# Performance work log

Hardware: AMD Instinct MI355X
Metric: run time of the kernel (lower is better)

Reference implementation:

```python
import jax, jax.numpy as jnp
import numpy as np
from jax import lax

B, E, D, N, R, K = 4, 768, 1536, 16, 48, 4
H, W = 16, 16
L = H * W
NDIR = 4


def _perms():
    idx = np.arange(L)
    idx_v = np.arange(L).reshape(H, W).T.reshape(-1)  # column-major (vertical) scan order
    perms = [idx, idx[::-1].copy(), idx_v, idx_v[::-1].copy()]
    invs = [np.argsort(p) for p in perms]
    return [jnp.asarray(p) for p in perms], [jnp.asarray(p) for p in invs]

PERMS, INVS = _perms()


def setup_inputs() -> dict:
    key = jax.random.key(0)
    ks = jax.random.split(key, 10)
    hidden_states = jax.random.normal(ks[0], (B, L, E), jnp.float32)
    in_proj_w = jax.random.normal(ks[1], (2 * D, E), jnp.float32) * 0.02
    out_proj_w = jax.random.normal(ks[2], (E, D), jnp.float32) * 0.02
    conv_w = jax.random.normal(ks[3], (NDIR, D, K), jnp.float32) * 0.1
    conv_b = jax.random.normal(ks[4], (NDIR, D), jnp.float32) * 0.1
    xproj_w = jax.random.normal(ks[5], (NDIR, R + 2 * N, D), jnp.float32) * 0.02
    dt_init_std = R ** -0.5
    dtproj_w = jax.random.uniform(ks[6], (NDIR, D, R), jnp.float32, -dt_init_std, dt_init_std)
    dt = jnp.exp(jax.random.uniform(ks[7], (NDIR, D), jnp.float32)
                 * (np.log(0.1) - np.log(0.001)) + np.log(0.001))
    dt = jnp.clip(dt, 1e-4, None)
    dtproj_b = dt + jnp.log(-jnp.expm1(-dt))  # inverse-softplus init as in the module
    A_log = jnp.broadcast_to(
        jnp.log(jnp.arange(1, N + 1, dtype=jnp.float32))[None, None, :], (NDIR, D, N)).copy()
    D_param = jnp.ones((NDIR, D), jnp.float32)
    return dict(hidden_states=hidden_states, in_proj_w=in_proj_w, out_proj_w=out_proj_w,
                conv_w=conv_w, conv_b=conv_b, xproj_w=xproj_w, dtproj_w=dtproj_w,
                dtproj_b=dtproj_b, A_log=A_log, D_param=D_param)


def _mamba_dir(xz, cw, cb, xw, dtw, dtb, a_log, dpar):
    # xz: (B, 2D, L) in this direction's scan order
    x, z = xz[:, :D], xz[:, D:]
    # causal depthwise conv1d + SiLU (mamba_inner_fn conv path)
    x = lax.conv_general_dilated(x, cw[:, None, :], (1,), [(K - 1, 0)],
                                 feature_group_count=D,
                                 dimension_numbers=('NCH', 'OIH', 'NCH'))
    x = jax.nn.silu(x + cb[None, :, None])
    # x_proj -> dt, B, C
    x_dbl = jnp.einsum('bdl,kd->bkl', x, xw)
    dt, Bm, Cm = x_dbl[:, :R], x_dbl[:, R:R + N], x_dbl[:, R + N:]
    delta = jax.nn.softplus(jnp.einsum('brl,dr->bdl', dt, dtw) + dtb[None, :, None])
    A = -jnp.exp(a_log)                                  # (D, N)
    dA = jnp.exp(jnp.einsum('bdl,dn->lbdn', delta, A))   # (L, B, D, N)
    dBu = jnp.einsum('bdl,bnl,bdl->lbdn', delta, Bm, x)  # delta * B * u

    def step(h, inp):
        da, dbu = inp
        h = da * h + dbu
        return h, h

    h0 = jnp.zeros((x.shape[0], D, N), x.dtype)
    _, hs = lax.scan(step, h0, (dA, dBu))                # (L, B, D, N)
    y = jnp.einsum('lbdn,bnl->bdl', hs, Cm) + dpar[None, :, None] * x
    return y * jax.nn.silu(z)                            # gate, (B, D, L)


def reference(hidden_states, in_proj_w, out_proj_w, conv_w, conv_b,
              xproj_w, dtproj_w, dtproj_b, A_log, D_param):
    xz = jnp.einsum('ble,fe->bfl', hidden_states, in_proj_w)  # (B, 2D, L)
    out = jnp.zeros((hidden_states.shape[0], D, L), hidden_states.dtype)
    for i in range(NDIR):  # fixed small set of structurally distinct scan directions
        xz_i = xz[:, :, PERMS[i]]
        y = _mamba_dir(xz_i, conv_w[i], conv_b[i], xproj_w[i], dtproj_w[i],
                       dtproj_b[i], A_log[i], D_param[i])
        out = out + y[:, :, INVS[i]]  # multi_reverse then sum-fusion
    return jnp.einsum('bdl,ed->ble', out, out_proj_w)
```

## Files before the change

### kernel.cpp

```cpp
#include <hip/hip_runtime.h>
#include <hip/hip_bf16.h>

#define BI   4
#define LI   256
#define EI   768
#define DI   1536
#define NI   16
#define RI   48
#define KI   4
#define NDIRS 4
#define F2D  3072
#define MROWS 1024
#define LOG2E 1.4426950408889634f
#define LN2   0.6931471805599453f

typedef float    floatx2 __attribute__((ext_vector_type(2)));
typedef float    floatx4 __attribute__((ext_vector_type(4)));
typedef _Float16 halfx2  __attribute__((ext_vector_type(2)));
typedef _Float16 halfx4  __attribute__((ext_vector_type(4)));
typedef _Float16 halfx8  __attribute__((ext_vector_type(8)));

typedef __attribute__((address_space(3))) unsigned lds_u32;
typedef __attribute__((address_space(1))) const unsigned glb_u32;

__device__ __forceinline__ void load16(const _Float16* g, _Float16* l) {
    __builtin_amdgcn_global_load_lds((glb_u32*)g, (lds_u32*)l, 16, 0, 0);
}

__device__ __forceinline__ int perm_idx(int dir, int j) {
    switch (dir) {
        case 0:  return j;
        case 1:  return 255 - j;
        case 2:  return ((j & 15) << 4) | (j >> 4);
        default: return 255 - (((j & 15) << 4) | (j >> 4));
    }
}

template<int CTRL>
__device__ __forceinline__ float dpp_add(float p) {
    int t = __builtin_amdgcn_update_dpp(0, __builtin_bit_cast(int, p),
                                        CTRL, 0xf, 0xf, true);
    return p + __builtin_bit_cast(float, t);
}
__device__ __forceinline__ float grp8_sum(float p) {
    p = dpp_add<0xB1>(p);
    p = dpp_add<0x4E>(p);
    p = dpp_add<0x141>(p);
    return p;
}

template<int BM, int BN, int WGN, int FM, int FN, int VM>
__device__ __forceinline__ void gemm_core(const _Float16* __restrict__ Ah,
                                          const _Float16* __restrict__ Al, int lda,
                                          const _Float16* __restrict__ Bh,
                                          const _Float16* __restrict__ Bl, int ldb,
                                          int nChunks, _Float16* smem,
                                          floatx4 (&acc)[FM][FN]) {
    const int tid = threadIdx.x, lane = tid & 63, wave = tid >> 6;
    const int wave_m = wave / WGN, wave_n = wave % WGN;
    const int rr = lane & 15, koff = (lane >> 4) * 8;
    const int arow = wave_m * FM * 16, brow = wave_n * FN * 16;
    constexpr int BUFSZ = (BM + BN) * 64;

    auto stage = [&](int c, int bf) {
        _Float16* sAh = smem + bf * BUFSZ;
        _Float16* sAl = sAh + BM * 32;
        _Float16* sBh = sAh + BM * 64;
        _Float16* sBl = sAh + BM * 64 + BN * 32;
        for (int idx = tid; idx < BM * 4; idx += 256) {
            int r = idx >> 2, s = (idx & 3) * 8;
            load16(Ah + (size_t)r * lda + c * 32 + s, sAh + idx * 8);
            load16(Al + (size_t)r * lda + c * 32 + s, sAl + idx * 8);
        }
        for (int idx = tid; idx < BN * 4; idx += 256) {
            int r = idx >> 2, s = (idx & 3) * 8;
            load16(Bh + (size_t)r * ldb + c * 32 + s, sBh + idx * 8);
            load16(Bl + (size_t)r * ldb + c * 32 + s, sBl + idx * 8);
        }
    };

    stage(0, 0);

    for (int c = 0; c < nChunks; ++c) {
        const int bf = c & 1;
        if (c + 1 < nChunks) {
            stage(c + 1, bf ^ 1);
            asm volatile("s_waitcnt vmcnt(%0)" :: "n"(VM) : "memory");
        } else {
            asm volatile("s_waitcnt vmcnt(0)" ::: "memory");
        }
        __builtin_amdgcn_s_barrier();

        const _Float16* sAh = smem + bf * BUFSZ;
        const _Float16* sAl = sAh + BM * 32;
        const _Float16* sBh = sAh + BM * 64;
        const _Float16* sBl = sAh + BM * 64 + BN * 32;
        halfx8 ahf[FM], alf[FM], bhf[FN], blf[FN];
        #pragma unroll
        for (int i = 0; i < FM; ++i) {
            ahf[i] = *(const halfx8*)(sAh + (arow + i * 16 + rr) * 32 + koff);
            alf[i] = *(const halfx8*)(sAl + (arow + i * 16 + rr) * 32 + koff);
        }
        #pragma unroll
        for (int j = 0; j < FN; ++j) {
            bhf[j] = *(const halfx8*)(sBh + (brow + j * 16 + rr) * 32 + koff);
            blf[j] = *(const halfx8*)(sBl + (brow + j * 16 + rr) * 32 + koff);
        }
        #pragma unroll
        for (int i = 0; i < FM; ++i)
            #pragma unroll
            for (int j = 0; j < FN; ++j) {
                acc[i][j] = __builtin_amdgcn_mfma_f32_16x16x32_f16(ahf[i], bhf[j], acc[i][j], 0, 0, 0);
                acc[i][j] = __builtin_amdgcn_mfma_f32_16x16x32_f16(ahf[i], blf[j], acc[i][j], 0, 0, 0);
                acc[i][j] = __builtin_amdgcn_mfma_f32_16x16x32_f16(alf[i], bhf[j], acc[i][j], 0, 0, 0);
            }
        asm volatile("s_waitcnt lgkmcnt(0)" ::: "memory");
        __builtin_amdgcn_s_barrier();
    }
}

__global__ __launch_bounds__(256) void k_splitall(
        const float* __restrict__ hs,  const float* __restrict__ wip,
        const float* __restrict__ wop, const float* __restrict__ xw,
        const float* __restrict__ dtw,
        _Float16* __restrict__ hsh,  _Float16* __restrict__ hsl,
        _Float16* __restrict__ wiph, _Float16* __restrict__ wipl,
        _Float16* __restrict__ woph, _Float16* __restrict__ wopl,
        _Float16* __restrict__ xwh,  _Float16* __restrict__ xwl,
        _Float16* __restrict__ dtwh, _Float16* __restrict__ dtwl) {
    int i4 = (blockIdx.x * 256 + threadIdx.x) * 4;
    floatx4 v;
    _Float16 *dh, *dl; int off;
    if (i4 < 786432)        { off = i4;           v = *(const floatx4*)(hs + off);  dh = hsh;  dl = hsl;  }
    else if (i4 < 3145728)  { off = i4 - 786432;  v = *(const floatx4*)(wip + off); dh = wiph; dl = wipl; }
    else if (i4 < 4325376)  { off = i4 - 3145728; v = *(const floatx4*)(wop + off); dh = woph; dl = wopl; }
    else if (i4 < 4816896)  { off = i4 - 4325376; v = *(const floatx4*)(xw + off);  dh = xwh;  dl = xwl;  }
    else {
        int t0 = i4 - 4816896;
        int col = t0 & 63, dr = t0 >> 6;
        floatx4 z = {0.f, 0.f, 0.f, 0.f};
        v = (col < 48) ? *(const floatx4*)(dtw + (size_t)dr * 48 + col) : z;
        dh = dtwh; dl = dtwl; off = t0;
    }
    halfx4 hh, hl;
    #pragma unroll
    for (int e = 0; e < 4; ++e) {
        _Float16 h = (_Float16)v[e];
        hh[e] = h; hl[e] = (_Float16)(v[e] - (float)h);
    }
    *(halfx4*)(dh + off) = hh;
    *(halfx4*)(dl + off) = hl;
}

__global__ __launch_bounds__(256) void k_inproj_t(const _Float16* __restrict__ Ah,
                                                  const _Float16* __restrict__ Al,
                                                  const _Float16* __restrict__ Bh,
                                                  const _Float16* __restrict__ Bl,
                                                  float* __restrict__ C) {
    __shared__ _Float16 smem[2 * 192 * 64];
    int row0 = blockIdx.x * 64, col0 = blockIdx.y * 128;
    floatx4 acc[2][4] = {};
    gemm_core<64, 128, 2, 2, 4, 6>(Ah + (size_t)row0 * EI, Al + (size_t)row0 * EI, EI,
                                   Bh + (size_t)col0 * EI, Bl + (size_t)col0 * EI, EI,
                                   24, smem, acc);
    int lane = threadIdx.x & 63, wave = threadIdx.x >> 6;
    int cc = lane & 15, q = lane >> 4;
    int rbase = row0 + (wave >> 1) * 32, cbase = col0 + (wave & 1) * 64;
    #pragma unroll
    for (int i = 0; i < 2; ++i)
        #pragma unroll
        for (int j = 0; j < 4; ++j)
            #pragma unroll
            for (int r = 0; r < 4; ++r)
                C[(size_t)(rbase + i * 16 + q * 4 + r) * F2D + cbase + j * 16 + cc] = acc[i][j][r];
}

__global__ __launch_bounds__(256) void k_outproj_t(const _Float16* __restrict__ Ah,
                                                   const _Float16* __restrict__ Al,
                                                   const _Float16* __restrict__ Bh,
                                                   const _Float16* __restrict__ Bl,
                                                   float* __restrict__ C) {
    __shared__ _Float16 smem[2 * 192 * 64];
    int row0 = blockIdx.x * 64, col0 = blockIdx.y * 128, k0 = blockIdx.z * 384;
    float* Cp = C + (size_t)blockIdx.z * MROWS * EI;
    floatx4 acc[2][4] = {};
    gemm_core<64, 128, 2, 2, 4, 6>(Ah + (size_t)row0 * DI + k0, Al + (size_t)row0 * DI + k0, DI,
                                   Bh + (size_t)col0 * DI + k0, Bl + (size_t)col0 * DI + k0, DI,
                                   12, smem, acc);
    int lane = threadIdx.x & 63, wave = threadIdx.x >> 6;
    int cc = lane & 15, q = lane >> 4;
    int rbase = row0 + (wave >> 1) * 32, cbase = col0 + (wave & 1) * 64;
    #pragma unroll
    for (int i = 0; i < 2; ++i)
        #pragma unroll
        for (int j = 0; j < 4; ++j)
            #pragma unroll
            for (int r = 0; r < 4; ++r)
                Cp[(size_t)(rbase + i * 16 + q * 4 + r) * EI + cbase + j * 16 + cc] = acc[i][j][r];
}

__global__ __launch_bounds__(256) void k_osum(const float* __restrict__ oacc,
                                              float* __restrict__ out) {
    int i4 = (blockIdx.x * 256 + threadIdx.x) * 4;
    const size_t S = (size_t)MROWS * EI;
    floatx4 s = *(const floatx4*)(oacc + i4) + *(const floatx4*)(oacc + S + i4) +
                *(const floatx4*)(oacc + 2 * S + i4) + *(const floatx4*)(oacc + 3 * S + i4);
    *(floatx4*)(out + i4) = s;
}

__global__ __launch_bounds__(256) void k_xdbl_t(const _Float16* __restrict__ xh,
                                                const _Float16* __restrict__ xl,
                                                const _Float16* __restrict__ xwh,
                                                const _Float16* __restrict__ xwl,
                                                float* __restrict__ C) {
    __shared__ _Float16 smem[2 * 144 * 64];
    int row0 = blockIdx.x * 64, dir = blockIdx.y, k0 = blockIdx.z * 192;
    float* Cp = C + (size_t)blockIdx.z * NDIRS * MROWS * 80;
    floatx4 acc[1][5] = {};
    const size_t abase = ((size_t)dir * MROWS + row0) * DI + k0;
    const size_t bbase = (size_t)dir * 80 * DI + k0;
    gemm_core<64, 80, 1, 1, 5, 4>(xh + abase, xl + abase, DI,
                                  xwh + bbase, xwl + bbase, DI, 6, smem, acc);
    int lane = threadIdx.x & 63, wave = threadIdx.x >> 6;
    int cc = lane & 15, q = lane >> 4;
    int rbase = row0 + wave * 16;
    #pragma unroll
    for (int j = 0; j < 5; ++j)
        #pragma unroll
        for (int r = 0; r < 4; ++r)
            Cp[((size_t)dir * MROWS + rbase + q * 4 + r) * 80 + j * 16 + cc] = acc[0][j][r];
}

__global__ __launch_bounds__(256) void k_xsplit(const float* __restrict__ acc,
                                                _Float16* __restrict__ dtqh,
                                                _Float16* __restrict__ dtql,
                                                float* __restrict__ BCm) {
    const size_t PS = (size_t)NDIRS * MROWS * 80;
    int idx = blockIdx.x * 256 + threadIdx.x;
    int dir = idx / (MROWS * 96);
    int rem = idx - dir * MROWS * 96;
    int row = rem / 96, col = rem - row * 96;
    size_t rbase = (size_t)dir * MROWS + row;
    auto sum8 = [&](int c) {
        size_t o = rbase * 80 + c;
        float s = 0.f;
        #pragma unroll
        for (int kp = 0; kp < 8; ++kp) s += acc[kp * PS + o];
        return s;
    };
    if (col < 64) {
        float v = (col < 48) ? sum8(col) : 0.f;
        _Float16 h = (_Float16)v;
        dtqh[rbase * 64 + col] = h;
        dtql[rbase * 64 + col] = (_Float16)(v - (float)h);
    } else if (col < 80) {
        int n = col - 64;
        BCm[rbase * 32 + (n >> 1) * 4 + (n & 1)] = sum8(48 + n);
    } else {
        int n = col - 80;
        BCm[rbase * 32 + (n >> 1) * 4 + 2 + (n & 1)] = sum8(64 + n);
    }
}

__global__ __launch_bounds__(512) void k_conv4(const float* __restrict__ xz,
                                               const float* __restrict__ cw,
                                               const float* __restrict__ cb,
                                               _Float16* __restrict__ xh,
                                               _Float16* __restrict__ xl) {
    const int b = blockIdx.y, d0 = blockIdx.x * 16;
    const int tid = threadIdx.x;
    __shared__ float sx[256][18];

    for (int i = tid; i < 1024; i += 512) {
        int row = i >> 2, c4 = (i & 3) * 4;
        size_t o = ((size_t)b * 256 + row) * F2D + d0 + c4;
        floatx4 v = *(const floatx4*)(xz + o);
        floatx2 v0 = {v[0], v[1]}, v1 = {v[2], v[3]};
        *(floatx2*)&sx[row][c4]     = v0;
        *(floatx2*)&sx[row][c4 + 2] = v1;
    }
    __syncthreads();

    const int dsub = tid & 15, lg = tid >> 4;
    const int d = d0 + dsub, j0 = lg * 8;
    #pragma unroll
    for (int dir = 0; dir < NDIRS; ++dir) {
        floatx4 w = *(const floatx4*)(cw + ((size_t)dir * DI + d) * KI);
        float bias = cb[(size_t)dir * DI + d];
        float xm3 = (j0 >= 3) ? sx[perm_idx(dir, j0 - 3)][dsub] : 0.f;
        float xm2 = (j0 >= 2) ? sx[perm_idx(dir, j0 - 2)][dsub] : 0.f;
        float xm1 = (j0 >= 1) ? sx[perm_idx(dir, j0 - 1)][dsub] : 0.f;
        #pragma unroll
        for (int j = 0; j < 8; ++j) {
            float cur = sx[perm_idx(dir, j0 + j)][dsub];
            float s = bias + w[0] * xm3 + w[1] * xm2 + w[2] * xm1 + w[3] * cur;
            xm3 = xm2; xm2 = xm1; xm1 = cur;
            float x = s / (1.f + __expf(-s));
            _Float16 h = (_Float16)x;
            size_t o = ((size_t)dir * MROWS + b * 256 + j0 + j) * DI + d;
            xh[o] = h;
            xl[o] = (_Float16)(x - (float)h);
        }
    }
}

__global__ __launch_bounds__(256) void k_scan(const _Float16* __restrict__ dtqh,
                                              const _Float16* __restrict__ dtql,
                                              const _Float16* __restrict__ dtwh,
                                              const _Float16* __restrict__ dtwl,
                                              const float* __restrict__ dtb,
                                              const _Float16* __restrict__ xhg,
                                              const _Float16* __restrict__ xlg,
                                              const float* __restrict__ BCm,
                                              const float* __restrict__ A_log,
                                              const float* __restrict__ Dp,
                                              float* __restrict__ ydir) {
    const int dchunk = blockIdx.x, b = blockIdx.y, dir = blockIdx.z;
    const int tid = threadIdx.x, lane = tid & 63, wave = tid >> 6;
    const int dslot = tid >> 3;
    const int np = tid & 7;
    const int d0 = dchunk * 32, d = d0 + dslot;

    __shared__ float sdx[2][32][68];
    __shared__ float sbc[2][32][32];
    __shared__ float sY[2][32][32];

    const floatx2 Av = {
        -__expf(A_log[((size_t)dir * DI + d) * NI + 2 * np]) * LOG2E,
        -__expf(A_log[((size_t)dir * DI + d) * NI + 2 * np + 1]) * LOG2E };
    const float Dpar = Dp[(size_t)dir * DI + d];
    floatx2 h = {0.f, 0.f};

    const size_t dirrow = (size_t)dir * MROWS;
    const int srow = tid >> 3, sc4 = (tid & 7) * 4;

    const int rowhalf = wave >> 1, dhalf = wave & 1;
    const int rr = lane & 15, koff = (lane >> 4) * 8, q = lane >> 4;
    const size_t bfb = ((size_t)dir * DI + d0 + dhalf * 16 + rr) * 64;
    halfx8 bhf[2], blf[2];
    bhf[0] = *(const halfx8*)(dtwh + bfb + koff);
    bhf[1] = *(const halfx8*)(dtwh + bfb + 32 + koff);
    blf[0] = *(const halfx8*)(dtwl + bfb + koff);
    blf[1] = *(const halfx8*)(dtwl + bfb + 32 + koff);
    const float bias = dtb[(size_t)dir * DI + d0 + dhalf * 16 + rr];

    floatx4 rbc;
    halfx4 rxh, rxl;
    auto load_chunk = [&](int j0) {
        int row = b * 256 + j0 + srow;
        size_t o = (dirrow + row) * DI + d0 + sc4;
        rxh = *(const halfx4*)(xhg + o);
        rxl = *(const halfx4*)(xlg + o);
        rbc = *(const floatx4*)(BCm + (dirrow + row) * 32 + sc4);
    };
    halfx8 ahf[2], alf[2];
    auto load_afrag = [&](int c) {
        size_t o = (dirrow + b * 256 + c * 32 + rowhalf * 16 + rr) * 64;
        ahf[0] = *(const halfx8*)(dtqh + o + koff);
        ahf[1] = *(const halfx8*)(dtqh + o + 32 + koff);
        alf[0] = *(const halfx8*)(dtql + o + koff);
        alf[1] = *(const halfx8*)(dtql + o + 32 + koff);
    };
    auto stage = [&](int bf) {
        #pragma unroll
        for (int e = 0; e < 4; ++e)
            sdx[bf][sc4 + e][srow * 2 + 1] = (float)rxh[e] + (float)rxl[e];
        *(floatx4*)&sbc[bf][srow][sc4] = rbc;
    };
    auto mfma_delta = [&](int bf) {
        floatx4 acc = {};
        #pragma unroll
        for (int kc = 0; kc < 2; ++kc) {
            acc = __builtin_amdgcn_mfma_f32_16x16x32_f16(ahf[kc], bhf[kc], acc, 0, 0, 0);
            acc = __builtin_amdgcn_mfma_f32_16x16x32_f16(ahf[kc], blf[kc], acc, 0, 0, 0);
            acc = __builtin_amdgcn_mfma_f32_16x16x32_f16(alf[kc], bhf[kc], acc, 0, 0, 0);
        }
        #pragma unroll
        for (int r = 0; r < 4; ++r) {
            float v = acc[r] + bias;
            float sp = (v > 20.f) ? v
                     : __log2f(1.f + __builtin_amdgcn_exp2f(v * LOG2E)) * LN2;
            sdx[bf][dhalf * 16 + rr][(rowhalf * 16 + q * 4 + r) * 2] = sp;
        }
    };

    load_chunk(0);
    load_afrag(0);
    stage(0);
    mfma_delta(0);
    load_chunk(32);
    load_afrag(1);
    __syncthreads();

    for (int c = 0; c < 8; ++c) {
        const int buf = c & 1;
        if (c < 7) {
            stage(buf ^ 1);
            mfma_delta(buf ^ 1);
            if (c < 6) { load_chunk((c + 2) * 32); load_afrag(c + 2); }
        }

        __builtin_amdgcn_s_setprio(1);
        #pragma unroll
        for (int g = 0; g < 4; ++g) {
            floatx4 dxr[4], bcr[8];
            #pragma unroll
            for (int k = 0; k < 4; ++k)
                dxr[k] = *(const floatx4*)&sdx[buf][dslot][(g * 8 + k * 2) * 2];
            #pragma unroll
            for (int k = 0; k < 8; ++k)
                bcr[k] = *(const floatx4*)&sbc[buf][g * 8 + k][np * 4];
            float yv[8];
            #pragma unroll
            for (int k = 0; k < 8; ++k) {
                float dv = dxr[k >> 1][(k & 1) * 2], xv = dxr[k >> 1][(k & 1) * 2 + 1];
                floatx4 bc = bcr[k];
                floatx2 tt = Av * dv;
                floatx2 a = { __builtin_amdgcn_exp2f(tt[0]),
                              __builtin_amdgcn_exp2f(tt[1]) };
                float du = dv * xv;
                floatx2 Bp = { bc[0], bc[1] };
                floatx2 Cp = { bc[2], bc[3] };
                h = __builtin_elementwise_fma(a, h, Bp * du);
                floatx2 qv = h * Cp;
                float p = qv[0] + qv[1];
                p = grp8_sum(p);
                yv[k] = fmaf(Dpar, xv, p);
            }
            if (np == 0) {
                #pragma unroll
                for (int k = 0; k < 8; ++k)
                    sY[buf][g * 8 + k][dslot] = yv[k];
            }
        }
        __builtin_amdgcn_s_setprio(0);
        __syncthreads();

        {
            int lout = perm_idx(dir, c * 32 + srow);
            floatx4 o = *(const floatx4*)&sY[buf][srow][sc4];
            *(floatx4*)&ydir[(dirrow + (size_t)b * 256 + lout) * DI + d0 + sc4] = o;
        }
    }
}

__global__ __launch_bounds__(256) void k_sum(const float* __restrict__ ydir,
                                             const float* __restrict__ xz,
                                             _Float16* __restrict__ yh,
                                             _Float16* __restrict__ yl) {
    int i4 = (blockIdx.x * 256 + threadIdx.x) * 4;
    const size_t S = (size_t)MROWS * DI;
    int row = i4 / DI, dcol = i4 - row * DI;
    size_t zo = (size_t)row * F2D + DI + dcol;
    floatx4 zv = *(const floatx4*)(xz + zo);
    floatx4 s = *(const floatx4*)(ydir + i4) + *(const floatx4*)(ydir + S + i4) +
                *(const floatx4*)(ydir + 2 * S + i4) + *(const floatx4*)(ydir + 3 * S + i4);
    halfx4 hh, hl;
    #pragma unroll
    for (int e = 0; e < 4; ++e) {
        float g = zv[e] / (1.f + __expf(-zv[e]));
        float v = s[e] * g;
        _Float16 h = (_Float16)v;
        hh[e] = h; hl[e] = (_Float16)(v - (float)h);
    }
    *(halfx4*)(yh + i4) = hh;
    *(halfx4*)(yl + i4) = hl;
}

extern "C" void kernel_launch(void* const* d_in, const int* in_sizes, int n_in,
                              void* d_out, int out_size, void* d_ws, size_t ws_size,
                              hipStream_t stream) {
    const float* hs   = (const float*)d_in[0];
    const float* wip  = (const float*)d_in[1];
    const float* wop  = (const float*)d_in[2];
    const float* cw   = (const float*)d_in[3];
    const float* cb   = (const float*)d_in[4];
    const float* xw   = (const float*)d_in[5];
    const float* dtw  = (const float*)d_in[6];
    const float* dtb  = (const float*)d_in[7];
    const float* alog = (const float*)d_in[8];
    const float* dpar = (const float*)d_in[9];
    float* out = (float*)d_out;

    char* p = (char*)d_ws;
    auto alloc_f32 = [&](size_t n) { float* r = (float*)p; p += n * 4; return r; };
    auto alloc_f16 = [&](size_t n) { _Float16* r = (_Float16*)p; p += n * 2; return r; };

    _Float16* hsh  = alloc_f16(786432);
    _Float16* hsl  = alloc_f16(786432);
    _Float16* wiph = alloc_f16(2359296);
    _Float16* wipl = alloc_f16(2359296);
    _Float16* woph = alloc_f16(1179648);
    _Float16* wopl = alloc_f16(1179648);
    _Float16* xwh  = alloc_f16(491520);
    _Float16* xwl  = alloc_f16(491520);
    _Float16* dtwh = alloc_f16((size_t)NDIRS * DI * 64);
    _Float16* dtwl = alloc_f16((size_t)NDIRS * DI * 64);
    float*    xz   = alloc_f32((size_t)MROWS * F2D);
    _Float16* xh   = alloc_f16((size_t)NDIRS * MROWS * DI);
    _Float16* xl   = alloc_f16((size_t)NDIRS * MROWS * DI);
    _Float16* dtqh = alloc_f16((size_t)NDIRS * MROWS * 64);
    _Float16* dtql = alloc_f16((size_t)NDIRS * MROWS * 64);
    float*    BCm  = alloc_f32((size_t)NDIRS * MROWS * 32);
    float*    oacc = alloc_f32((size_t)4 * MROWS * EI);
    float*    ydir = alloc_f32((size_t)NDIRS * MROWS * DI);
    _Float16* yh   = alloc_f16((size_t)MROWS * DI);
    _Float16* yl   = alloc_f16((size_t)MROWS * DI);

    float* xdba = ydir;

    k_splitall<<<dim3(5088), 256, 0, stream>>>(hs, wip, wop, xw, dtw,
                                               hsh, hsl, wiph, wipl, woph, wopl,
                                               xwh, xwl, dtwh, dtwl);
    k_inproj_t<<<dim3(16, 24), 256, 0, stream>>>(hsh, hsl, wiph, wipl, xz);
    k_conv4   <<<dim3(96, BI), 512, 0, stream>>>(xz, cw, cb, xh, xl);
    k_xdbl_t  <<<dim3(16, NDIRS, 8), 256, 0, stream>>>(xh, xl, xwh, xwl, xdba);
    k_xsplit  <<<dim3(1536), 256, 0, stream>>>(xdba, dtqh, dtql, BCm);
    k_scan    <<<dim3(DI / 32, BI, NDIRS), 256, 0, stream>>>(dtqh, dtql, dtwh, dtwl, dtb,
                                                             xh, xl, BCm, alog, dpar, ydir);
    k_sum     <<<dim3(1536), 256, 0, stream>>>(ydir, xz, yh, yl);
    k_outproj_t<<<dim3(16, 6, 4), 256, 0, stream>>>(yh, yl, woph, wopl, oacc);
    k_osum    <<<dim3(768), 256, 0, stream>>>(oacc, out);
}
```

Measured before the change: 197.8 us.

## Assign one SSM state per thread in scan kernel, halve channels per block

The selective-scan kernel now gives each thread a single state element (16 threads per channel) instead of two, and each block covers 16 channels instead of 32. The grid doubles to 1536 blocks. This shortens each thread's serial recurrence work and raises parallelism across the GPU. In exchange it adds a fourth DPP reduction step, leaves two of the four waves idle during the delta MFMA, and makes global loads and stores narrower.

```diff
diff --git a/kernel.cpp b/kernel.cpp
--- a/kernel.cpp
+++ b/kernel.cpp
@@ -42,10 +42,11 @@
                                         CTRL, 0xf, 0xf, true);
     return p + __builtin_bit_cast(float, t);
 }
-__device__ __forceinline__ float grp8_sum(float p) {
+__device__ __forceinline__ float grp16_sum(float p) {
     p = dpp_add<0xB1>(p);
     p = dpp_add<0x4E>(p);
     p = dpp_add<0x141>(p);
+    p = dpp_add<0x140>(p);
     return p;
 }
 
@@ -317,45 +318,45 @@
                                               float* __restrict__ ydir) {
     const int dchunk = blockIdx.x, b = blockIdx.y, dir = blockIdx.z;
     const int tid = threadIdx.x, lane = tid & 63, wave = tid >> 6;
-    const int dslot = tid >> 3;
-    const int np = tid & 7;
-    const int d0 = dchunk * 32, d = d0 + dslot;
-
-    __shared__ float sdx[2][32][68];
+    const int dslot = tid >> 4;
+    const int np = tid & 15;
+    const int d0 = dchunk * 16, d = d0 + dslot;
+
+    __shared__ float sdx[2][16][68];
     __shared__ float sbc[2][32][32];
-    __shared__ float sY[2][32][32];
-
-    const floatx2 Av = {
-        -__expf(A_log[((size_t)dir * DI + d) * NI + 2 * np]) * LOG2E,
-        -__expf(A_log[((size_t)dir * DI + d) * NI + 2 * np + 1]) * LOG2E };
+    __shared__ float sY[2][32][20];
+
+    const float Av = -__expf(A_log[((size_t)dir * DI + d) * NI + np]) * LOG2E;
     const float Dpar = Dp[(size_t)dir * DI + d];
-    floatx2 h = {0.f, 0.f};
+    float h = 0.f;
 
     const size_t dirrow = (size_t)dir * MROWS;
-    const int srow = tid >> 3, sc4 = (tid & 7) * 4;
-
-    const int rowhalf = wave >> 1, dhalf = wave & 1;
+    const int srow = tid >> 3, sc2 = (tid & 7) * 2, sc4 = (tid & 7) * 4;
+
     const int rr = lane & 15, koff = (lane >> 4) * 8, q = lane >> 4;
-    const size_t bfb = ((size_t)dir * DI + d0 + dhalf * 16 + rr) * 64;
     halfx8 bhf[2], blf[2];
-    bhf[0] = *(const halfx8*)(dtwh + bfb + koff);
-    bhf[1] = *(const halfx8*)(dtwh + bfb + 32 + koff);
-    blf[0] = *(const halfx8*)(dtwl + bfb + koff);
-    blf[1] = *(const halfx8*)(dtwl + bfb + 32 + koff);
-    const float bias = dtb[(size_t)dir * DI + d0 + dhalf * 16 + rr];
+    float bias = 0.f;
+    if (wave < 2) {
+        const size_t bfb = ((size_t)dir * DI + d0 + rr) * 64;
+        bhf[0] = *(const halfx8*)(dtwh + bfb + koff);
+        bhf[1] = *(const halfx8*)(dtwh + bfb + 32 + koff);
+        blf[0] = *(const halfx8*)(dtwl + bfb + koff);
+        blf[1] = *(const halfx8*)(dtwl + bfb + 32 + koff);
+        bias = dtb[(size_t)dir * DI + d0 + rr];
+    }
 
     floatx4 rbc;
-    halfx4 rxh, rxl;
+    halfx2 rxh, rxl;
     auto load_chunk = [&](int j0) {
         int row = b * 256 + j0 + srow;
-        size_t o = (dirrow + row) * DI + d0 + sc4;
-        rxh = *(const halfx4*)(xhg + o);
-        rxl = *(const halfx4*)(xlg + o);
+        size_t o = (dirrow + row) * DI + d0 + sc2;
+        rxh = *(const halfx2*)(xhg + o);
+        rxl = *(const halfx2*)(xlg + o);
         rbc = *(const floatx4*)(BCm + (dirrow + row) * 32 + sc4);
     };
     halfx8 ahf[2], alf[2];
     auto load_afrag = [&](int c) {
-        size_t o = (dirrow + b * 256 + c * 32 + rowhalf * 16 + rr) * 64;
+        size_t o = (dirrow + b * 256 + c * 32 + wave * 16 + rr) * 64;
         ahf[0] = *(const halfx8*)(dtqh + o + koff);
         ahf[1] = *(const halfx8*)(dtqh + o + 32 + koff);
         alf[0] = *(const halfx8*)(dtql + o + koff);
@@ -363,8 +364,8 @@
     };
     auto stage = [&](int bf) {
         #pragma unroll
-        for (int e = 0; e < 4; ++e)
-            sdx[bf][sc4 + e][srow * 2 + 1] = (float)rxh[e] + (float)rxl[e];
+        for (int e = 0; e < 2; ++e)
+            sdx[bf][sc2 + e][srow * 2 + 1] = (float)rxh[e] + (float)rxl[e];
         *(floatx4*)&sbc[bf][srow][sc4] = rbc;
     };
     auto mfma_delta = [&](int bf) {
@@ -380,24 +381,24 @@
             float v = acc[r] + bias;
             float sp = (v > 20.f) ? v
                      : __log2f(1.f + __builtin_amdgcn_exp2f(v * LOG2E)) * LN2;
-            sdx[bf][dhalf * 16 + rr][(rowhalf * 16 + q * 4 + r) * 2] = sp;
+            sdx[bf][rr][(wave * 16 + q * 4 + r) * 2] = sp;
         }
     };
 
     load_chunk(0);
-    load_afrag(0);
+    if (wave < 2) load_afrag(0);
     stage(0);
-    mfma_delta(0);
+    if (wave < 2) mfma_delta(0);
     load_chunk(32);
-    load_afrag(1);
+    if (wave < 2) load_afrag(1);
     __syncthreads();
 
     for (int c = 0; c < 8; ++c) {
         const int buf = c & 1;
         if (c < 7) {
             stage(buf ^ 1);
-            mfma_delta(buf ^ 1);
-            if (c < 6) { load_chunk((c + 2) * 32); load_afrag(c + 2); }
+            if (wave < 2) mfma_delta(buf ^ 1);
+            if (c < 6) { load_chunk((c + 2) * 32); if (wave < 2) load_afrag(c + 2); }
         }
 
         __builtin_amdgcn_s_setprio(1);
@@ -409,22 +410,16 @@
                 dxr[k] = *(const floatx4*)&sdx[buf][dslot][(g * 8 + k * 2) * 2];
             #pragma unroll
             for (int k = 0; k < 8; ++k)
-                bcr[k] = *(const floatx4*)&sbc[buf][g * 8 + k][np * 4];
+                bcr[k] = *(const floatx4*)&sbc[buf][g * 8 + k][(np >> 1) * 4];
             float yv[8];
             #pragma unroll
             for (int k = 0; k < 8; ++k) {
                 float dv = dxr[k >> 1][(k & 1) * 2], xv = dxr[k >> 1][(k & 1) * 2 + 1];
-                floatx4 bc = bcr[k];
-                floatx2 tt = Av * dv;
-                floatx2 a = { __builtin_amdgcn_exp2f(tt[0]),
-                              __builtin_amdgcn_exp2f(tt[1]) };
+                float Bv = bcr[k][np & 1], Cv = bcr[k][2 + (np & 1)];
+                float a = __builtin_amdgcn_exp2f(dv * Av);
                 float du = dv * xv;
-                floatx2 Bp = { bc[0], bc[1] };
-                floatx2 Cp = { bc[2], bc[3] };
-                h = __builtin_elementwise_fma(a, h, Bp * du);
-                floatx2 qv = h * Cp;
-                float p = qv[0] + qv[1];
-                p = grp8_sum(p);
+                h = fmaf(a, h, Bv * du);
+                float p = grp16_sum(h * Cv);
                 yv[k] = fmaf(Dpar, xv, p);
             }
             if (np == 0) {
@@ -438,8 +433,8 @@
 
         {
             int lout = perm_idx(dir, c * 32 + srow);
-            floatx4 o = *(const floatx4*)&sY[buf][srow][sc4];
-            *(floatx4*)&ydir[(dirrow + (size_t)b * 256 + lout) * DI + d0 + sc4] = o;
+            floatx2 o = *(const floatx2*)&sY[buf][srow][sc2];
+            *(floatx2*)&ydir[(dirrow + (size_t)b * 256 + lout) * DI + d0 + sc2] = o;
         }
     }
 }
@@ -516,7 +511,7 @@
     k_conv4   <<<dim3(96, BI), 512, 0, stream>>>(xz, cw, cb, xh, xl);
     k_xdbl_t  <<<dim3(16, NDIRS, 8), 256, 0, stream>>>(xh, xl, xwh, xwl, xdba);
     k_xsplit  <<<dim3(1536), 256, 0, stream>>>(xdba, dtqh, dtql, BCm);
-    k_scan    <<<dim3(DI / 32, BI, NDIRS), 256, 0, stream>>>(dtqh, dtql, dtwh, dtwl, dtb,
+    k_scan    <<<dim3(DI / 16, BI, NDIRS), 256, 0, stream>>>(dtqh, dtql, dtwh, dtwl, dtb,
                                                              xh, xl, BCm, alog, dpar, ydir);
     k_sum     <<<dim3(1536), 256, 0, stream>>>(ydir, xz, yh, yl);
     k_outproj_t<<<dim3(16, 6, 4), 256, 0, stream>>>(yh, yl, woph, wopl, oacc);
```

After: 230.4 us. 1.16x slower.
